# Optimization experiments

Hardware: AMD Instinct MI355X
Metric: run time of the kernel (lower is better)

Reference implementation:

```python
import jax, jax.numpy as jnp
import numpy as np

FOCAL_LENGTH = 1000.0
IMG_SIZE = 512.0
EPS = 1e-8


def setup_inputs() -> dict:
    key = jax.random.key(0)
    ks = jax.random.split(key, 11)
    B, J, V = 512, 24, 6890
    return {
        "pred_rotmat": jax.random.normal(ks[0], (B, J, 3, 3), jnp.float32),
        "pred_camera": jax.random.uniform(ks[1], (B, 3), jnp.float32, 0.2, 1.0),
        "pred_joints": jax.random.normal(ks[2], (B, J, 3), jnp.float32),
        "pred_vertices": jax.random.normal(ks[3], (B, V, 3), jnp.float32),
        "pred_betas": jax.random.normal(ks[4], (B, 10), jnp.float32),
        "gt_rotmat": jax.random.normal(ks[5], (B, J, 3, 3), jnp.float32),
        "gt_shape": jax.random.normal(ks[6], (B, 10), jnp.float32),
        "gt_keypoints_2d": jax.random.uniform(ks[7], (B, J, 3), jnp.float32),
        "gt_keypoints_3d": jax.random.uniform(ks[8], (B, J, 4), jnp.float32),
        "gt_vertices": jax.random.normal(ks[9], (B, V, 3), jnp.float32),
        "has_smpl": jax.random.randint(ks[10], (B,), 0, 2, jnp.int32),
    }


def _procrustes_align(S1, S2):
    # S1, S2: [B, N, 3] -> similarity transform of S1 onto S2 (batched closed-form Procrustes)
    S1 = jnp.swapaxes(S1, 1, 2)  # [B,3,N]
    S2 = jnp.swapaxes(S2, 1, 2)
    mu1 = jnp.mean(S1, axis=-1, keepdims=True)
    mu2 = jnp.mean(S2, axis=-1, keepdims=True)
    X1 = S1 - mu1
    X2 = S2 - mu2
    var1 = jnp.sum(X1 * X1, axis=(1, 2))  # [B]
    K = jnp.matmul(X1, jnp.swapaxes(X2, 1, 2)) + EPS  # [B,3,3]
    U, s, Vh = jnp.linalg.svd(K)
    Vt = Vh  # torch V^T == jax Vh
    sign = jnp.sign(jnp.linalg.det(jnp.matmul(U, Vt)))  # det(U @ V^T)
    Z = jnp.broadcast_to(jnp.eye(3, dtype=S1.dtype), K.shape)
    Z = Z.at[:, -1, -1].multiply(sign)
    R = jnp.matmul(jnp.swapaxes(Vh, 1, 2), jnp.matmul(Z, jnp.swapaxes(U, 1, 2)))
    scale = jnp.trace(jnp.matmul(R, K), axis1=1, axis2=2) / var1  # [B]
    t = mu2 - scale[:, None, None] * jnp.matmul(R, mu1)
    S1_hat = scale[:, None, None] * jnp.matmul(R, S1) + t
    return jnp.swapaxes(S1_hat, 1, 2), jnp.swapaxes(S2, 1, 2)


def reference(pred_rotmat, pred_camera, pred_joints, pred_vertices, pred_betas,
              gt_rotmat, gt_shape, gt_keypoints_2d, gt_keypoints_3d, gt_vertices,
              has_smpl):
    B = pred_joints.shape[0]
    f = jnp.float32(FOCAL_LENGTH)
    img = jnp.float32(IMG_SIZE)

    # --- perspective projection with identity rotation ---
    depth = 2.0 * f / (EPS + pred_camera[:, 0] * img)  # [B]
    translation = jnp.stack([pred_camera[:, 1], pred_camera[:, 2], depth], axis=-1)  # [B,3]
    pts = pred_joints + translation[:, None, :]  # [B,J,3]
    pred_kp2d = f * pts[..., :2] / pts[..., 2:3] + img / 2.0  # [B,J,2]

    # --- 2D keypoint loss (normalized by image size, confidence weighted L1) ---
    pred_kp2d_n = pred_kp2d / img
    gt_kp2d_n = gt_keypoints_2d[..., :2] / img
    conf2d = gt_keypoints_2d[..., 2:]
    loss_kp2d = jnp.mean(conf2d * jnp.abs(pred_kp2d_n - gt_kp2d_n))

    # --- 3D keypoint loss (pelvis-aligned, confidence weighted L1) ---
    conf3d = gt_keypoints_3d[..., 3:]
    gt3 = gt_keypoints_3d[..., :3]
    gt_pelvis = (gt3[:, 2:3] + gt3[:, 3:4]) / 2.0
    pr_pelvis = (pred_joints[:, 2:3] + pred_joints[:, 3:4]) / 2.0
    loss_kp3d = jnp.mean(conf3d * jnp.abs((pred_joints - pr_pelvis) - (gt3 - gt_pelvis)))

    # --- masked shape / SMPL parameter losses ---
    mask = (has_smpl > 0).astype(pred_vertices.dtype)  # [B]
    n_valid = jnp.sum(mask)
    V = pred_vertices.shape[1]
    loss_shape = jnp.sum(mask[:, None, None] * jnp.abs(pred_vertices - gt_vertices)) / (n_valid * V * 3 + EPS)
    loss_pose = jnp.sum(mask[:, None, None, None] * (pred_rotmat - gt_rotmat) ** 2) / (n_valid * 24 * 9 + EPS)
    loss_betas = jnp.sum(mask[:, None] * (pred_betas - gt_shape) ** 2) / (n_valid * 10 + EPS)

    # --- PA-MPJPE via batched 3x3 SVD Procrustes (eval-only in original: no grad) ---
    S1_hat, S2 = _procrustes_align(pred_joints, gt3)
    pa_mpjpe = jnp.mean(jnp.sqrt(jnp.sum((S1_hat - S2) ** 2, axis=-1)))

    total = (4.0 * loss_kp2d + 4.0 * loss_kp3d + loss_shape + loss_pose
             + 0.01 * loss_betas + jax.lax.stop_gradient(pa_mpjpe))
    return total
```

## Files before the change

### kernel.cpp

```cpp
#include <hip/hip_runtime.h>
#include <math.h>

#define EPSF   1e-8f
#define NV4    2645760
#define PER_B  20670

#define B_PROC   0
#define B_NV     8
#define B_BETA   10
#define B_KP2D   30
#define B_KP3D   78
#define B_POSE   126
#define B_VERT   234
#define NBLK     1526

__device__ __forceinline__ float frcp(float x)  { return __builtin_amdgcn_rcpf(x); }
__device__ __forceinline__ float frsq(float x)  { return __builtin_amdgcn_rsqf(x); }
__device__ __forceinline__ float fsqrt(float x) { return __builtin_amdgcn_sqrtf(x); }

__device__ __forceinline__ void block_sum_store(float v, double* dst) {
  #pragma unroll
  for (int off = 32; off > 0; off >>= 1) v += __shfl_down(v, off);
  __shared__ float red[4];
  const int lane = threadIdx.x & 63;
  const int wid  = threadIdx.x >> 6;
  if (lane == 0) red[wid] = v;
  __syncthreads();
  if (threadIdx.x == 0) *dst = (double)(red[0] + red[1] + red[2] + red[3]);
}

template<int P, int Q>
__device__ __forceinline__ void jrot(float A[3][3], float Vv[3][3]) {
  float apq = A[P][Q];
  if (fabsf(apq) < 1e-20f) return;
  float tau = (A[Q][Q] - A[P][P]) * 0.5f * frcp(apq);
  float t   = copysignf(1.f, tau) * frcp(fabsf(tau) + fsqrt(1.f + tau * tau));
  float c   = frsq(1.f + t * t);
  float s   = t * c;
  float cP[3], cQ[3];
  #pragma unroll
  for (int k = 0; k < 3; ++k) { cP[k] = c*A[k][P] - s*A[k][Q]; cQ[k] = s*A[k][P] + c*A[k][Q]; }
  #pragma unroll
  for (int k = 0; k < 3; ++k) { A[k][P] = cP[k]; A[k][Q] = cQ[k]; }
  float rP[3], rQ[3];
  #pragma unroll
  for (int k = 0; k < 3; ++k) { rP[k] = c*A[P][k] - s*A[Q][k]; rQ[k] = s*A[P][k] + c*A[Q][k]; }
  #pragma unroll
  for (int k = 0; k < 3; ++k) { A[P][k] = rP[k]; A[Q][k] = rQ[k]; }
  #pragma unroll
  for (int k = 0; k < 3; ++k) {
    float vp = c*Vv[k][P] - s*Vv[k][Q];
    Vv[k][Q] = s*Vv[k][P] + c*Vv[k][Q];
    Vv[k][P] = vp;
  }
}

#define CSWAP(I, J)                                                        \
  if (lam[I] < lam[J]) {                                                   \
    float tl = lam[I]; lam[I] = lam[J]; lam[J] = tl;                       \
    _Pragma("unroll")                                                      \
    for (int r = 0; r < 3; ++r) {                                          \
      float tv = Vv[r][I]; Vv[r][I] = Vv[r][J]; Vv[r][J] = tv;             \
    }                                                                      \
  }

__device__ float procrustes_err(const float4* __restrict__ P4,
                                const float4* __restrict__ G4, int b) {
  const float4* Pr = P4 + b * 18;
  const float4* Gr = G4 + b * 24;

  float sx0=0,sx1=0,sx2=0, sy0=0,sy1=0,sy2=0, sxx=0;
  float Ku[3][3] = {{0,0,0},{0,0,0},{0,0,0}};
  #pragma unroll
  for (int g = 0; g < 6; ++g) {
    float4 p0 = Pr[g*3+0], p1 = Pr[g*3+1], p2 = Pr[g*3+2];
    float px[4][3] = {{p0.x,p0.y,p0.z},{p0.w,p1.x,p1.y},
                      {p1.z,p1.w,p2.x},{p2.y,p2.z,p2.w}};
    #pragma unroll
    for (int q = 0; q < 4; ++q) {
      float4 gg = Gr[g*4+q];
      float x0 = px[q][0], x1 = px[q][1], x2 = px[q][2];
      sx0 += x0; sx1 += x1; sx2 += x2;
      sy0 += gg.x; sy1 += gg.y; sy2 += gg.z;
      sxx += x0*x0 + x1*x1 + x2*x2;
      Ku[0][0]+=x0*gg.x; Ku[0][1]+=x0*gg.y; Ku[0][2]+=x0*gg.z;
      Ku[1][0]+=x1*gg.x; Ku[1][1]+=x1*gg.y; Ku[1][2]+=x1*gg.z;
      Ku[2][0]+=x2*gg.x; Ku[2][1]+=x2*gg.y; Ku[2][2]+=x2*gg.z;
    }
  }
  const float inv24 = 1.f / 24.f;
  float mu1x=sx0*inv24, mu1y=sx1*inv24, mu1z=sx2*inv24;
  float mu2x=sy0*inv24, mu2y=sy1*inv24, mu2z=sy2*inv24;
  float m1v[3] = {mu1x, mu1y, mu1z};
  float m2v[3] = {mu2x, mu2y, mu2z};
  float K[3][3];
  #pragma unroll
  for (int r = 0; r < 3; ++r)
    #pragma unroll
    for (int c = 0; c < 3; ++c)
      K[r][c] = Ku[r][c] - 24.f * m1v[r] * m2v[c] + EPSF;
  float var1 = sxx - 24.f * (mu1x*mu1x + mu1y*mu1y + mu1z*mu1z);

  float detK = K[0][0]*(K[1][1]*K[2][2]-K[1][2]*K[2][1])
             - K[0][1]*(K[1][0]*K[2][2]-K[1][2]*K[2][0])
             + K[0][2]*(K[1][0]*K[2][1]-K[1][1]*K[2][0]);
  float sgn = (detK > 0.f) ? 1.f : ((detK < 0.f) ? -1.f : 0.f);

  float A[3][3];
  #pragma unroll
  for (int r = 0; r < 3; ++r)
    #pragma unroll
    for (int c = 0; c < 3; ++c)
      A[r][c] = K[0][r]*K[0][c] + K[1][r]*K[1][c] + K[2][r]*K[2][c];

  float Vv[3][3] = {{1,0,0},{0,1,0},{0,0,1}};
  for (int sweep = 0; sweep < 8; ++sweep) {
    jrot<0,1>(A, Vv); jrot<0,2>(A, Vv); jrot<1,2>(A, Vv);
  }
  float lam[3] = {A[0][0], A[1][1], A[2][2]};
  CSWAP(0,1) CSWAP(0,2) CSWAP(1,2)

  float Rm[3][3] = {{0,0,0},{0,0,0},{0,0,0}};
  float zi[3] = {1.f, 1.f, sgn};
  float trRK = 0.f;
  #pragma unroll
  for (int i = 0; i < 3; ++i) {
    float v0 = Vv[0][i], v1 = Vv[1][i], v2 = Vv[2][i];
    float a0 = K[0][0]*v0 + K[0][1]*v1 + K[0][2]*v2;
    float a1 = K[1][0]*v0 + K[1][1]*v1 + K[1][2]*v2;
    float a2 = K[2][0]*v0 + K[2][1]*v1 + K[2][2]*v2;
    float s2 = a0*a0 + a1*a1 + a2*a2;
    float si = fsqrt(s2);
    float zs = zi[i] * frcp(fmaxf(si, 1e-20f));
    Rm[0][0]+=zs*v0*a0; Rm[0][1]+=zs*v0*a1; Rm[0][2]+=zs*v0*a2;
    Rm[1][0]+=zs*v1*a0; Rm[1][1]+=zs*v1*a1; Rm[1][2]+=zs*v1*a2;
    Rm[2][0]+=zs*v2*a0; Rm[2][1]+=zs*v2*a1; Rm[2][2]+=zs*v2*a2;
    trRK += zi[i] * si;
  }
  float scale = trRK * frcp(var1);
  float t0 = mu2x - scale*(Rm[0][0]*mu1x + Rm[0][1]*mu1y + Rm[0][2]*mu1z);
  float t1 = mu2y - scale*(Rm[1][0]*mu1x + Rm[1][1]*mu1y + Rm[1][2]*mu1z);
  float t2 = mu2z - scale*(Rm[2][0]*mu1x + Rm[2][1]*mu1y + Rm[2][2]*mu1z);

  float errsum = 0.f;
  #pragma unroll
  for (int g = 0; g < 6; ++g) {
    float4 p0 = Pr[g*3+0], p1 = Pr[g*3+1], p2 = Pr[g*3+2];
    float px[4][3] = {{p0.x,p0.y,p0.z},{p0.w,p1.x,p1.y},
                      {p1.z,p1.w,p2.x},{p2.y,p2.z,p2.w}};
    #pragma unroll
    for (int q = 0; q < 4; ++q) {
      float4 gg = Gr[g*4+q];
      float X = px[q][0], Y = px[q][1], Z = px[q][2];
      float q0 = scale*(Rm[0][0]*X + Rm[0][1]*Y + Rm[0][2]*Z) + t0;
      float q1 = scale*(Rm[1][0]*X + Rm[1][1]*Y + Rm[1][2]*Z) + t1;
      float q2 = scale*(Rm[2][0]*X + Rm[2][1]*Y + Rm[2][2]*Z) + t2;
      float d0 = q0 - gg.x, d1 = q1 - gg.y, d2 = q2 - gg.z;
      errsum += fsqrt(d0*d0 + d1*d1 + d2*d2);
    }
  }
  return errsum;
}

__global__ __launch_bounds__(256) void bmp_main(
    const float4* __restrict__ pred_rot4,   const float* __restrict__ pred_camera,
    const float*  __restrict__ pred_joints, const float4* __restrict__ pred_verts,
    const float*  __restrict__ pred_betas,  const float4* __restrict__ gt_rot4,
    const float*  __restrict__ gt_shape,    const float* __restrict__ gt_kp2d,
    const float*  __restrict__ gt_kp3d,     const float4* __restrict__ gt_verts,
    const int*    __restrict__ has_smpl,    double* __restrict__ ws) {
  const int bid = blockIdx.x;
  const int tid = threadIdx.x;

  if (bid >= B_VERT) {
    const int chunk  = bid - B_VERT;
    const int f4base = chunk * 2048;
    const int nf4    = min(2048, NV4 - f4base);
    const int e0     = f4base * 4;
    const int b0     = e0 / PER_B;
    const int blast  = (e0 + nf4 * 4 - 1) / PER_B;
    const int m0     = has_smpl[b0] > 0;
    const int m1     = has_smpl[blast] > 0;
    float acc = 0.f;
    if (m0 | m1) {
      const float4* __restrict__ P = pred_verts + f4base + tid;
      const float4* __restrict__ G = gt_verts  + f4base + tid;
      if (nf4 == 2048) {
        float4 pa[8], ga[8];
        #pragma unroll
        for (int k = 0; k < 8; ++k) pa[k] = P[k * 256];
        #pragma unroll
        for (int k = 0; k < 8; ++k) ga[k] = G[k * 256];
        if (m0 & m1) {
          #pragma unroll
          for (int k = 0; k < 8; ++k)
            acc += fabsf(pa[k].x-ga[k].x) + fabsf(pa[k].y-ga[k].y)
                 + fabsf(pa[k].z-ga[k].z) + fabsf(pa[k].w-ga[k].w);
        } else {
          const int   bnd = (b0 + 1) * PER_B;
          const float fm0 = m0 ? 1.f : 0.f;
          const float fm1 = m1 ? 1.f : 0.f;
          #pragma unroll
          for (int k = 0; k < 8; ++k) {
            int e = (f4base + tid + k * 256) * 4;
            acc += ((e+0) >= bnd ? fm1 : fm0) * fabsf(pa[k].x-ga[k].x)
                 + ((e+1) >= bnd ? fm1 : fm0) * fabsf(pa[k].y-ga[k].y)
                 + ((e+2) >= bnd ? fm1 : fm0) * fabsf(pa[k].z-ga[k].z)
                 + ((e+3) >= bnd ? fm1 : fm0) * fabsf(pa[k].w-ga[k].w);
          }
        }
      } else {
        #pragma unroll
        for (int k = 0; k < 7; ++k) {
          float4 a = P[k * 256], b = G[k * 256];
          acc += fabsf(a.x-b.x) + fabsf(a.y-b.y) + fabsf(a.z-b.z) + fabsf(a.w-b.w);
        }
      }
    }
    block_sum_store(acc, &ws[bid]);
    return;
  }

  if (bid >= B_POSE) {
    int idx = (bid - B_POSE) * 256 + tid;
    int b   = idx / 54;
    float m = (has_smpl[b] > 0) ? 1.f : 0.f;
    float4 p = pred_rot4[idx], g = gt_rot4[idx];
    float dx = p.x-g.x, dy = p.y-g.y, dz = p.z-g.z, dw = p.w-g.w;
    block_sum_store(m * (dx*dx + dy*dy + dz*dz + dw*dw), &ws[bid]);
    return;
  }

  if (bid >= B_KP3D) {
    int idx = (bid - B_KP3D) * 256 + tid;
    int b = idx / 24, j = idx - (idx / 24) * 24;
    const float* PJ = pred_joints + b * 72;
    const float* G  = gt_kp3d + b * 96;
    float cf = G[j*4+3];
    float ssum = 0.f;
    #pragma unroll
    for (int c = 0; c < 3; ++c) {
      float prp = 0.5f * (PJ[2*3+c] + PJ[3*3+c]);
      float gtp = 0.5f * (G[2*4+c] + G[3*4+c]);
      ssum += fabsf((PJ[j*3+c] - prp) - (G[j*4+c] - gtp));
    }
    block_sum_store(cf * ssum, &ws[bid]);
    return;
  }

  if (bid >= B_KP2D) {
    int idx = (bid - B_KP2D) * 256 + tid;
    int b = idx / 24, j = idx - (idx / 24) * 24;
    float cam0 = pred_camera[b*3+0], cam1 = pred_camera[b*3+1], cam2 = pred_camera[b*3+2];
    float depth = 2.f * 1000.f / (EPSF + cam0 * 512.f);
    float px = pred_joints[(b*24+j)*3+0] + cam1;
    float py = pred_joints[(b*24+j)*3+1] + cam2;
    float pz = pred_joints[(b*24+j)*3+2] + depth;
    float kxn = (1000.f * px / pz + 256.f) * (1.f / 512.f);
    float kyn = (1000.f * py / pz + 256.f) * (1.f / 512.f);
    float gx = gt_kp2d[(b*24+j)*3+0] * (1.f / 512.f);
    float gy = gt_kp2d[(b*24+j)*3+1] * (1.f / 512.f);
    float cf = gt_kp2d[(b*24+j)*3+2];
    block_sum_store(cf * (fabsf(kxn - gx) + fabsf(kyn - gy)), &ws[bid]);
    return;
  }

  if (bid >= B_BETA) {
    int idx = (bid - B_BETA) * 256 + tid;
    int b = idx / 10;
    float m = (has_smpl[b] > 0) ? 1.f : 0.f;
    float d = pred_betas[idx] - gt_shape[idx];
    block_sum_store(m * d * d, &ws[bid]);
    return;
  }

  if (bid >= B_NV) {
    int idx = (bid - B_NV) * 256 + tid;
    block_sum_store((has_smpl[idx] > 0) ? 1.f : 0.f, &ws[bid]);
    return;
  }

  {
    float e = 0.f;
    if (tid < 64) {
      int b = bid * 64 + tid;
      e = procrustes_err((const float4*)pred_joints, (const float4*)gt_kp3d, b);
    }
    block_sum_store(e, &ws[bid]);
  }
}

__global__ __launch_bounds__(256) void bmp_finalize(const double* __restrict__ ws,
                                                    float* __restrict__ out) {
  const int tid = threadIdx.x;
  double s[7] = {0,0,0,0,0,0,0};
  for (int i = tid; i < NBLK; i += 256) {
    double v = ws[i];
    int slot;
    if      (i >= B_VERT) slot = 0;
    else if (i >= B_POSE) slot = 1;
    else if (i >= B_KP3D) slot = 2;
    else if (i >= B_KP2D) slot = 3;
    else if (i >= B_BETA) slot = 4;
    else if (i >= B_NV)   slot = 5;
    else                  slot = 6;
    s[slot] += v;
  }
  #pragma unroll
  for (int k = 0; k < 7; ++k)
    #pragma unroll
    for (int off = 32; off > 0; off >>= 1) s[k] += __shfl_down(s[k], off);
  __shared__ double red[4][7];
  const int lane = tid & 63, wid = tid >> 6;
  if (lane == 0)
    #pragma unroll
    for (int k = 0; k < 7; ++k) red[wid][k] = s[k];
  __syncthreads();
  if (tid == 0) {
    double t[7];
    #pragma unroll
    for (int k = 0; k < 7; ++k) t[k] = red[0][k]+red[1][k]+red[2][k]+red[3][k];
    double nv = t[5];
    double loss_kp2d  = t[3] / 24576.0;
    double loss_kp3d  = t[2] / 36864.0;
    double loss_shape = t[0] / (nv * 20670.0 + 1e-8);
    double loss_pose  = t[1] / (nv * 216.0   + 1e-8);
    double loss_betas = t[4] / (nv * 10.0    + 1e-8);
    double pa         = t[6] / 12288.0;
    out[0] = (float)(4.0*loss_kp2d + 4.0*loss_kp3d + loss_shape + loss_pose
                     + 0.01*loss_betas + pa);
  }
}

extern "C" void kernel_launch(void* const* d_in, const int* in_sizes, int n_in,
                              void* d_out, int out_size, void* d_ws, size_t ws_size,
                              hipStream_t stream) {
  const float4* pred_rot4   = (const float4*)d_in[0];
  const float*  pred_camera = (const float*)d_in[1];
  const float*  pred_joints = (const float*)d_in[2];
  const float4* pred_verts  = (const float4*)d_in[3];
  const float*  pred_betas  = (const float*)d_in[4];
  const float4* gt_rot4     = (const float4*)d_in[5];
  const float*  gt_shape    = (const float*)d_in[6];
  const float*  gt_kp2d     = (const float*)d_in[7];
  const float*  gt_kp3d     = (const float*)d_in[8];
  const float4* gt_verts    = (const float4*)d_in[9];
  const int*    has_smpl    = (const int*)d_in[10];
  double* ws = (double*)d_ws;

  bmp_main<<<NBLK, 256, 0, stream>>>(pred_rot4, pred_camera, pred_joints,
      pred_verts, pred_betas, gt_rot4, gt_shape, gt_kp2d, gt_kp3d, gt_verts,
      has_smpl, ws);
  bmp_finalize<<<1, 256, 0, stream>>>(ws, (float*)d_out);
}
```

Before: 128.2 us.

## Split vertex L1 reduction into its own kernel with tighter register budget

Moves the large vertex-difference reduction out of the monolithic kernel into a dedicated kernel with launch_bounds(256,8), and loads in two halves of four float4 pairs instead of eight at once. This is meant to lower register pressure so more waves stay resident for the bandwidth-bound stream, free of the heavy Procrustes/SVD code that inflated the combined kernel's register count. The side losses run in a second launch on the same stream, which adds launch overhead and serialises them after the vertex pass. It also adds a redundant store in the Jacobi rotation (A[P==Q?0:P]) that is a no-op for P!=Q.

```diff
diff --git a/kernel.cpp b/kernel.cpp
--- a/kernel.cpp
+++ b/kernel.cpp
@@ -4,15 +4,16 @@
 #define EPSF   1e-8f
 #define NV4    2645760
 #define PER_B  20670
-
-#define B_PROC   0
-#define B_NV     8
-#define B_BETA   10
-#define B_KP2D   30
-#define B_KP3D   78
-#define B_POSE   126
-#define B_VERT   234
-#define NBLK     1526
+#define NVBLK  1292
+
+#define S_PROC   0
+#define S_NV     8
+#define S_BETA   10
+#define S_KP2D   30
+#define S_KP3D   78
+#define S_POSE   126
+#define NSIDE    234
+#define NWS      (NVBLK + NSIDE)
 
 __device__ __forceinline__ float frcp(float x)  { return __builtin_amdgcn_rcpf(x); }
 __device__ __forceinline__ float frsq(float x)  { return __builtin_amdgcn_rsqf(x); }
@@ -27,6 +28,68 @@
   if (lane == 0) red[wid] = v;
   __syncthreads();
   if (threadIdx.x == 0) *dst = (double)(red[0] + red[1] + red[2] + red[3]);
+}
+
+__global__ __launch_bounds__(256, 8) void bmp_vert(
+    const float4* __restrict__ pred_verts, const float4* __restrict__ gt_verts,
+    const int*    __restrict__ has_smpl,   double* __restrict__ ws) {
+  const int bid = blockIdx.x;
+  const int tid = threadIdx.x;
+  const int f4base = bid * 2048;
+  const int nf4    = min(2048, NV4 - f4base);
+  const int e0     = f4base * 4;
+  const int b0     = e0 / PER_B;
+  const int blast  = (e0 + nf4 * 4 - 1) / PER_B;
+  const int m0     = has_smpl[b0] > 0;
+  const int m1     = has_smpl[blast] > 0;
+  float acc = 0.f;
+  if (m0 | m1) {
+    const float4* __restrict__ P = pred_verts + f4base + tid;
+    const float4* __restrict__ G = gt_verts  + f4base + tid;
+    if (nf4 == 2048) {
+      if (m0 & m1) {
+        #pragma unroll
+        for (int h = 0; h < 2; ++h) {
+          float4 pa[4], ga[4];
+          #pragma unroll
+          for (int k = 0; k < 4; ++k) pa[k] = P[(h * 4 + k) * 256];
+          #pragma unroll
+          for (int k = 0; k < 4; ++k) ga[k] = G[(h * 4 + k) * 256];
+          #pragma unroll
+          for (int k = 0; k < 4; ++k)
+            acc += fabsf(pa[k].x-ga[k].x) + fabsf(pa[k].y-ga[k].y)
+                 + fabsf(pa[k].z-ga[k].z) + fabsf(pa[k].w-ga[k].w);
+        }
+      } else {
+        const int   bnd = (b0 + 1) * PER_B;
+        const float fm0 = m0 ? 1.f : 0.f;
+        const float fm1 = m1 ? 1.f : 0.f;
+        #pragma unroll
+        for (int h = 0; h < 2; ++h) {
+          float4 pa[4], ga[4];
+          #pragma unroll
+          for (int k = 0; k < 4; ++k) pa[k] = P[(h * 4 + k) * 256];
+          #pragma unroll
+          for (int k = 0; k < 4; ++k) ga[k] = G[(h * 4 + k) * 256];
+          #pragma unroll
+          for (int k = 0; k < 4; ++k) {
+            int e = (f4base + tid + (h * 4 + k) * 256) * 4;
+            acc += ((e+0) >= bnd ? fm1 : fm0) * fabsf(pa[k].x-ga[k].x)
+                 + ((e+1) >= bnd ? fm1 : fm0) * fabsf(pa[k].y-ga[k].y)
+                 + ((e+2) >= bnd ? fm1 : fm0) * fabsf(pa[k].z-ga[k].z)
+                 + ((e+3) >= bnd ? fm1 : fm0) * fabsf(pa[k].w-ga[k].w);
+          }
+        }
+      }
+    } else {
+      #pragma unroll
+      for (int k = 0; k < 7; ++k) {
+        float4 a = P[k * 256], b = G[k * 256];
+        acc += fabsf(a.x-b.x) + fabsf(a.y-b.y) + fabsf(a.z-b.z) + fabsf(a.w-b.w);
+      }
+    }
+  }
+  block_sum_store(acc, &ws[bid]);
 }
 
 template<int P, int Q>
@@ -46,7 +109,7 @@
   #pragma unroll
   for (int k = 0; k < 3; ++k) { rP[k] = c*A[P][k] - s*A[Q][k]; rQ[k] = s*A[P][k] + c*A[Q][k]; }
   #pragma unroll
-  for (int k = 0; k < 3; ++k) { A[P][k] = rP[k]; A[Q][k] = rQ[k]; }
+  for (int k = 0; k < 3; ++k) { A[P][k] = rP[k]; A[P==Q?0:P][k] = rP[k]; A[Q][k] = rQ[k]; }
   #pragma unroll
   for (int k = 0; k < 3; ++k) {
     float vp = c*Vv[k][P] - s*Vv[k][Q];
@@ -129,8 +192,7 @@
     float a0 = K[0][0]*v0 + K[0][1]*v1 + K[0][2]*v2;
     float a1 = K[1][0]*v0 + K[1][1]*v1 + K[1][2]*v2;
     float a2 = K[2][0]*v0 + K[2][1]*v1 + K[2][2]*v2;
-    float s2 = a0*a0 + a1*a1 + a2*a2;
-    float si = fsqrt(s2);
+    float si = fsqrt(a0*a0 + a1*a1 + a2*a2);
     float zs = zi[i] * frcp(fmaxf(si, 1e-20f));
     Rm[0][0]+=zs*v0*a0; Rm[0][1]+=zs*v0*a1; Rm[0][2]+=zs*v0*a2;
     Rm[1][0]+=zs*v1*a0; Rm[1][1]+=zs*v1*a1; Rm[1][2]+=zs*v1*a2;
@@ -162,77 +224,27 @@
   return errsum;
 }
 
-__global__ __launch_bounds__(256) void bmp_main(
+__global__ __launch_bounds__(256) void bmp_side(
     const float4* __restrict__ pred_rot4,   const float* __restrict__ pred_camera,
-    const float*  __restrict__ pred_joints, const float4* __restrict__ pred_verts,
-    const float*  __restrict__ pred_betas,  const float4* __restrict__ gt_rot4,
-    const float*  __restrict__ gt_shape,    const float* __restrict__ gt_kp2d,
-    const float*  __restrict__ gt_kp3d,     const float4* __restrict__ gt_verts,
+    const float*  __restrict__ pred_joints, const float* __restrict__ pred_betas,
+    const float4* __restrict__ gt_rot4,     const float* __restrict__ gt_shape,
+    const float*  __restrict__ gt_kp2d,     const float* __restrict__ gt_kp3d,
     const int*    __restrict__ has_smpl,    double* __restrict__ ws) {
   const int bid = blockIdx.x;
   const int tid = threadIdx.x;
-
-  if (bid >= B_VERT) {
-    const int chunk  = bid - B_VERT;
-    const int f4base = chunk * 2048;
-    const int nf4    = min(2048, NV4 - f4base);
-    const int e0     = f4base * 4;
-    const int b0     = e0 / PER_B;
-    const int blast  = (e0 + nf4 * 4 - 1) / PER_B;
-    const int m0     = has_smpl[b0] > 0;
-    const int m1     = has_smpl[blast] > 0;
-    float acc = 0.f;
-    if (m0 | m1) {
-      const float4* __restrict__ P = pred_verts + f4base + tid;
-      const float4* __restrict__ G = gt_verts  + f4base + tid;
-      if (nf4 == 2048) {
-        float4 pa[8], ga[8];
-        #pragma unroll
-        for (int k = 0; k < 8; ++k) pa[k] = P[k * 256];
-        #pragma unroll
-        for (int k = 0; k < 8; ++k) ga[k] = G[k * 256];
-        if (m0 & m1) {
-          #pragma unroll
-          for (int k = 0; k < 8; ++k)
-            acc += fabsf(pa[k].x-ga[k].x) + fabsf(pa[k].y-ga[k].y)
-                 + fabsf(pa[k].z-ga[k].z) + fabsf(pa[k].w-ga[k].w);
-        } else {
-          const int   bnd = (b0 + 1) * PER_B;
-          const float fm0 = m0 ? 1.f : 0.f;
-          const float fm1 = m1 ? 1.f : 0.f;
-          #pragma unroll
-          for (int k = 0; k < 8; ++k) {
-            int e = (f4base + tid + k * 256) * 4;
-            acc += ((e+0) >= bnd ? fm1 : fm0) * fabsf(pa[k].x-ga[k].x)
-                 + ((e+1) >= bnd ? fm1 : fm0) * fabsf(pa[k].y-ga[k].y)
-                 + ((e+2) >= bnd ? fm1 : fm0) * fabsf(pa[k].z-ga[k].z)
-                 + ((e+3) >= bnd ? fm1 : fm0) * fabsf(pa[k].w-ga[k].w);
-          }
-        }
-      } else {
-        #pragma unroll
-        for (int k = 0; k < 7; ++k) {
-          float4 a = P[k * 256], b = G[k * 256];
-          acc += fabsf(a.x-b.x) + fabsf(a.y-b.y) + fabsf(a.z-b.z) + fabsf(a.w-b.w);
-        }
-      }
-    }
-    block_sum_store(acc, &ws[bid]);
-    return;
-  }
-
-  if (bid >= B_POSE) {
-    int idx = (bid - B_POSE) * 256 + tid;
+  double* dst = &ws[NVBLK + bid];
+
+  if (bid >= S_POSE) {
+    int idx = (bid - S_POSE) * 256 + tid;
     int b   = idx / 54;
     float m = (has_smpl[b] > 0) ? 1.f : 0.f;
     float4 p = pred_rot4[idx], g = gt_rot4[idx];
     float dx = p.x-g.x, dy = p.y-g.y, dz = p.z-g.z, dw = p.w-g.w;
-    block_sum_store(m * (dx*dx + dy*dy + dz*dz + dw*dw), &ws[bid]);
-    return;
-  }
-
-  if (bid >= B_KP3D) {
-    int idx = (bid - B_KP3D) * 256 + tid;
+    block_sum_store(m * (dx*dx + dy*dy + dz*dz + dw*dw), dst);
+    return;
+  }
+  if (bid >= S_KP3D) {
+    int idx = (bid - S_KP3D) * 256 + tid;
     int b = idx / 24, j = idx - (idx / 24) * 24;
     const float* PJ = pred_joints + b * 72;
     const float* G  = gt_kp3d + b * 96;
@@ -244,12 +256,11 @@
       float gtp = 0.5f * (G[2*4+c] + G[3*4+c]);
       ssum += fabsf((PJ[j*3+c] - prp) - (G[j*4+c] - gtp));
     }
-    block_sum_store(cf * ssum, &ws[bid]);
-    return;
-  }
-
-  if (bid >= B_KP2D) {
-    int idx = (bid - B_KP2D) * 256 + tid;
+    block_sum_store(cf * ssum, dst);
+    return;
+  }
+  if (bid >= S_KP2D) {
+    int idx = (bid - S_KP2D) * 256 + tid;
     int b = idx / 24, j = idx - (idx / 24) * 24;
     float cam0 = pred_camera[b*3+0], cam1 = pred_camera[b*3+1], cam2 = pred_camera[b*3+2];
     float depth = 2.f * 1000.f / (EPSF + cam0 * 512.f);
@@ -261,32 +272,29 @@
     float gx = gt_kp2d[(b*24+j)*3+0] * (1.f / 512.f);
     float gy = gt_kp2d[(b*24+j)*3+1] * (1.f / 512.f);
     float cf = gt_kp2d[(b*24+j)*3+2];
-    block_sum_store(cf * (fabsf(kxn - gx) + fabsf(kyn - gy)), &ws[bid]);
-    return;
-  }
-
-  if (bid >= B_BETA) {
-    int idx = (bid - B_BETA) * 256 + tid;
+    block_sum_store(cf * (fabsf(kxn - gx) + fabsf(kyn - gy)), dst);
+    return;
+  }
+  if (bid >= S_BETA) {
+    int idx = (bid - S_BETA) * 256 + tid;
     int b = idx / 10;
     float m = (has_smpl[b] > 0) ? 1.f : 0.f;
     float d = pred_betas[idx] - gt_shape[idx];
-    block_sum_store(m * d * d, &ws[bid]);
-    return;
-  }
-
-  if (bid >= B_NV) {
-    int idx = (bid - B_NV) * 256 + tid;
-    block_sum_store((has_smpl[idx] > 0) ? 1.f : 0.f, &ws[bid]);
-    return;
-  }
-
+    block_sum_store(m * d * d, dst);
+    return;
+  }
+  if (bid >= S_NV) {
+    int idx = (bid - S_NV) * 256 + tid;
+    block_sum_store((has_smpl[idx] > 0) ? 1.f : 0.f, dst);
+    return;
+  }
   {
     float e = 0.f;
     if (tid < 64) {
       int b = bid * 64 + tid;
       e = procrustes_err((const float4*)pred_joints, (const float4*)gt_kp3d, b);
     }
-    block_sum_store(e, &ws[bid]);
+    block_sum_store(e, dst);
   }
 }
 
@@ -294,16 +302,19 @@
                                                     float* __restrict__ out) {
   const int tid = threadIdx.x;
   double s[7] = {0,0,0,0,0,0,0};
-  for (int i = tid; i < NBLK; i += 256) {
+  for (int i = tid; i < NWS; i += 256) {
     double v = ws[i];
     int slot;
-    if      (i >= B_VERT) slot = 0;
-    else if (i >= B_POSE) slot = 1;
-    else if (i >= B_KP3D) slot = 2;
-    else if (i >= B_KP2D) slot = 3;
-    else if (i >= B_BETA) slot = 4;
-    else if (i >= B_NV)   slot = 5;
-    else                  slot = 6;
+    if (i < NVBLK) slot = 0;
+    else {
+      int j = i - NVBLK;
+      if      (j >= S_POSE) slot = 1;
+      else if (j >= S_KP3D) slot = 2;
+      else if (j >= S_KP2D) slot = 3;
+      else if (j >= S_BETA) slot = 4;
+      else if (j >= S_NV)   slot = 5;
+      else                  slot = 6;
+    }
     s[slot] += v;
   }
   #pragma unroll
@@ -348,8 +359,8 @@
   const int*    has_smpl    = (const int*)d_in[10];
   double* ws = (double*)d_ws;
 
-  bmp_main<<<NBLK, 256, 0, stream>>>(pred_rot4, pred_camera, pred_joints,
-      pred_verts, pred_betas, gt_rot4, gt_shape, gt_kp2d, gt_kp3d, gt_verts,
-      has_smpl, ws);
+  bmp_vert<<<NVBLK, 256, 0, stream>>>(pred_verts, gt_verts, has_smpl, ws);
+  bmp_side<<<NSIDE, 256, 0, stream>>>(pred_rot4, pred_camera, pred_joints,
+      pred_betas, gt_rot4, gt_shape, gt_kp2d, gt_kp3d, has_smpl, ws);
   bmp_finalize<<<1, 256, 0, stream>>>(ws, (float*)d_out);
 }
```

Result: slower. 136.8 us (+6.7%).
